# Optimization experiments

Hardware: AMD Instinct MI355X
Metric: run time of the kernel (lower is better)

The kernel has to match this reference:

```python
import jax, jax.numpy as jnp
import numpy as np

N_TREES, DEPTH, INPUT_DIM, N_CLASSES = 15, 3, 128, 10
N_LEAVES = 2 ** DEPTH
N_INTERNAL = N_LEAVES - 1


def _path_masks(depth):
    """Right/left ancestor indicator matrices [n_leaves, n_internal]."""
    n_leaves = 2 ** depth
    n_int = n_leaves - 1
    R = np.zeros((n_leaves, n_int), np.float32)
    L = np.zeros((n_leaves, n_int), np.float32)
    for leaf in range(n_leaves):
        node = leaf + n_int
        for _ in range(depth):
            parent = (node - 1) // 2
            if node % 2 == 0:
                R[leaf, parent] = 1.0
            else:
                L[leaf, parent] = 1.0
            node = parent
    return R, L

_R, _L = _path_masks(DEPTH)


def setup_inputs() -> dict:
    key = jax.random.key(0)
    k1, k2 = jax.random.split(key)
    batch = 262144
    per_tree = N_INTERNAL * INPUT_DIM + N_INTERNAL + N_LEAVES * N_CLASSES
    total = N_TREES * per_tree + N_TREES
    x = jax.random.normal(k1, (batch, INPUT_DIM), dtype=jnp.float32)
    params = jax.random.normal(k2, (total,), dtype=jnp.float32)
    return {"x": x, "params": params}


def reference(x, params):
    per_tree = N_INTERNAL * INPUT_DIM + N_INTERNAL + N_LEAVES * N_CLASSES
    blocks = params[: N_TREES * per_tree].reshape(N_TREES, per_tree)
    w_end = N_INTERNAL * INPUT_DIM
    split_w = blocks[:, :w_end].reshape(N_TREES, N_INTERNAL, INPUT_DIM)
    split_b = blocks[:, w_end : w_end + N_INTERNAL]  # [T, n_internal]
    leaf_logits = blocks[:, w_end + N_INTERNAL :].reshape(N_TREES, N_LEAVES, N_CLASSES)
    tree_w_logits = params[N_TREES * per_tree :]  # [T]

    # split logits z: [B, T, n_internal]
    z = jnp.einsum("bd,tnd->btn", x, split_w) + split_b[None, :, :]
    log_p = jax.nn.log_sigmoid(z)        # log sigma(z)
    log_1mp = jax.nn.log_sigmoid(-z)     # log (1 - sigma(z))

    R = jnp.asarray(_R)
    L = jnp.asarray(_L)
    # path product in log domain: [B, T, n_leaves]
    leaf_probs = jnp.exp(
        jnp.einsum("btn,ln->btl", log_p, R) + jnp.einsum("btn,ln->btl", log_1mp, L)
    )

    leaf_class_probs = jax.nn.softmax(leaf_logits, axis=-1)  # [T, n_leaves, C]
    tree_pred = jnp.einsum("btl,tlc->btc", leaf_probs, leaf_class_probs)
    tree_weights = jax.nn.softmax(tree_w_logits, axis=0)     # [T]
    final_pred = jnp.einsum("btc,t->bc", tree_pred, tree_weights)
    return final_pred
```

## Files before the change

kernel.cpp:

```cpp
#include <hip/hip_runtime.h>
#include <hip/hip_fp16.h>


typedef float    f32x4 __attribute__((ext_vector_type(4)));
typedef _Float16 half8 __attribute__((ext_vector_type(8)));

#define TREES      15
#define IDIM       128
#define NCLS       10
#define NINT       7
#define NLVS       8
#define PER_TREE   (NINT*IDIM + NINT + NLVS*NCLS)
#define NODES      (TREES*NINT)
#define NPAD       112
#define KPAD       128
#define RSTR       272
#define NBLK       512

__global__ __launch_bounds__(256) void prep_kernel(const float* __restrict__ p,
                                                   _Float16* __restrict__ wq,
                                                   float* __restrict__ bq,
                                                   _Float16* __restrict__ wbT) {
    const int gid  = blockIdx.x * 256 + threadIdx.x;
    const int nthr = gridDim.x * 256;

    for (int i = gid; i < NPAD * IDIM; i += nthr) {
        int g = i >> 7, k = i & 127;
        float v = 0.f;
        if (g < NODES) {
            int t = g / NINT, n = g % NINT;
            v = p[t * PER_TREE + n * IDIM + k];
        }
        wq[i] = (_Float16)v;
    }
    for (int i = gid; i < NPAD; i += nthr) {
        float v = 0.f;
        if (i < NODES) {
            int t = i / NINT, n = i % NINT;
            v = p[t * PER_TREE + NINT * IDIM + n];
        }
        bq[i] = v;
    }
    const float* tl = p + TREES * PER_TREE;
    for (int i = gid; i < 16 * KPAD; i += nthr) {
        int c = i >> 7, k = i & 127;
        float v = 0.f;
        if (c < NCLS && k < TREES * NLVS) {
            int t = k >> 3, l = k & 7;
            const float* ll = p + t * PER_TREE + NINT * IDIM + NINT + l * NCLS;
            float mx = ll[0];
            #pragma unroll
            for (int j = 1; j < NCLS; ++j) mx = fmaxf(mx, ll[j]);
            float se = 0.f;
            #pragma unroll
            for (int j = 0; j < NCLS; ++j) se += __expf(ll[j] - mx);
            float lsm = __expf(ll[c] - mx) / se;

            float m2 = tl[0];
            #pragma unroll
            for (int j = 1; j < TREES; ++j) m2 = fmaxf(m2, tl[j]);
            float s2 = 0.f;
            #pragma unroll
            for (int j = 0; j < TREES; ++j) s2 += __expf(tl[j] - m2);
            float tw = __expf(tl[t] - m2) / s2;
            v = lsm * tw;
        }
        wbT[i] = (_Float16)v;
    }
}

__device__ __forceinline__ void dma_quarter(const float* __restrict__ x,
                                            long grow0, char* qdst, int lane) {
    const int slot = lane & 31;
    #pragma unroll
    for (int it = 0; it < 8; ++it) {
        int r   = 2 * it + (lane >> 5);
        int c16 = (slot - r) & 31;
        const float* gp = x + (grow0 + r) * IDIM + c16 * 4;
        __builtin_amdgcn_global_load_lds(
            (const __attribute__((address_space(1))) void*)gp,
            (__attribute__((address_space(3))) void*)(qdst + it * 1024),
            16, 0, 0);
    }
}

__global__ __launch_bounds__(256, 2) void tree_main(const float* __restrict__ x,
                                                    const _Float16* __restrict__ wq,
                                                    const float* __restrict__ bq,
                                                    const _Float16* __restrict__ wbT,
                                                    float* __restrict__ out,
                                                    int tpb) {
    __shared__ __align__(16) char lds[2][32768];

    const int tid  = threadIdx.x;
    const int lane = tid & 63;
    const int w    = tid >> 6;
    const int lm   = lane & 15;
    const int lq   = lane >> 4;
    const int rg   = lane >> 2;
    const int g    = lane & 3;

    const long tile0 = (long)blockIdx.x * tpb;

    dma_quarter(x, tile0 * 64 + 16 * w, &lds[0][w * 8192], lane);

    half8 bf[7][4];
    float bb[7];
    #pragma unroll
    for (int nt = 0; nt < 7; ++nt) {
        bb[nt] = bq[16 * nt + lm];
        #pragma unroll
        for (int s = 0; s < 4; ++s)
            bf[nt][s] = *reinterpret_cast<const half8*>(wq + (16 * nt + lm) * IDIM + 32 * s + 8 * lq);
    }
    half8 wbf[4];
    #pragma unroll
    for (int s = 0; s < 4; ++s)
        wbf[s] = *reinterpret_cast<const half8*>(wbT + lm * KPAD + 32 * s + 8 * lq);

    for (int i = 0; i < tpb; ++i) {
        char* qcur = &lds[i & 1][w * 8192];
        const long grow = (tile0 + i) * 64;

        asm volatile("" ::: "memory");
        __builtin_amdgcn_s_waitcnt(0x0F70);
        asm volatile("" ::: "memory");

        half8 af[4];
        #pragma unroll
        for (int s = 0; s < 4; ++s) {
            int cc = 8 * s + 2 * lq;
            f32x4 f0 = *(const f32x4*)(qcur + lm * 512 + (((cc     + lm) & 31) << 4));
            f32x4 f1 = *(const f32x4*)(qcur + lm * 512 + (((cc + 1 + lm) & 31) << 4));
            half8 a;
            #pragma unroll
            for (int j = 0; j < 4; ++j) {
                a[j]     = (_Float16)f0[j];
                a[j + 4] = (_Float16)f1[j];
            }
            af[s] = a;
        }

        if (i + 1 < tpb)
            dma_quarter(x, (tile0 + i + 1) * 64 + 16 * w, &lds[(i + 1) & 1][w * 8192], lane);

        #pragma unroll
        for (int nt = 0; nt < 7; ++nt) {
            f32x4 acc = {0.f, 0.f, 0.f, 0.f};
            #pragma unroll
            for (int s = 0; s < 4; ++s)
                acc = __builtin_amdgcn_mfma_f32_16x16x32_f16(af[s], bf[nt][s], acc, 0, 0, 0);
            int node = 16 * nt + lm;
            int col  = node + ((node * 9363) >> 16);
            #pragma unroll
            for (int r = 0; r < 4; ++r) {
                float z  = acc[r] + bb[nt];
                float sg = __builtin_amdgcn_rcpf(1.0f + __expf(-z));
                *(_Float16*)(qcur + (4 * lq + r) * RSTR + col * 2) = (_Float16)sg;
            }
        }

        {
            const char* rowp = qcur + rg * RSTR;
            float sgv[4][7];
            #pragma unroll
            for (int tt = 0; tt < 4; ++tt) {
                int t = 4 * g + tt;
                #pragma unroll
                for (int n = 0; n < 7; ++n)
                    sgv[tt][n] = (float)*(const _Float16*)(rowp + (8 * t + n) * 2);
            }
            half8 lv[4];
            #pragma unroll
            for (int tt = 0; tt < 4; ++tt) {
                float s0 = sgv[tt][0], s1 = sgv[tt][1], s2 = sgv[tt][2];
                float s3 = sgv[tt][3], s4 = sgv[tt][4], s5 = sgv[tt][5], s6 = sgv[tt][6];
                float u1 = 1.f - s0, u2 = s0;
                float q1 = u1 * s1, q0 = u1 - q1;
                float q3 = u2 * s2, q2 = u2 - q3;
                float L1 = q0 * s3, L0 = q0 - L1;
                float L3 = q1 * s4, L2 = q1 - L3;
                float L5 = q2 * s5, L4 = q2 - L5;
                float L7 = q3 * s6, L6 = q3 - L7;
                float m = (4 * g + tt < TREES) ? 1.f : 0.f;
                half8 lv8;
                lv8[0] = (_Float16)(L0 * m); lv8[1] = (_Float16)(L1 * m);
                lv8[2] = (_Float16)(L2 * m); lv8[3] = (_Float16)(L3 * m);
                lv8[4] = (_Float16)(L4 * m); lv8[5] = (_Float16)(L5 * m);
                lv8[6] = (_Float16)(L6 * m); lv8[7] = (_Float16)(L7 * m);
                lv[tt] = lv8;
            }
            #pragma unroll
            for (int tt = 0; tt < 4; ++tt)
                *(half8*)(qcur + rg * RSTR + 64 * g + 16 * tt) = lv[tt];
        }

        {
            half8 af2[4];
            #pragma unroll
            for (int s = 0; s < 4; ++s)
                af2[s] = *(const half8*)(qcur + lm * RSTR + 64 * s + 16 * lq);
            f32x4 a2 = {0.f, 0.f, 0.f, 0.f};
            #pragma unroll
            for (int s = 0; s < 4; ++s)
                a2 = __builtin_amdgcn_mfma_f32_16x16x32_f16(af2[s], wbf[s], a2, 0, 0, 0);
            if (lm < NCLS) {
                #pragma unroll
                for (int r = 0; r < 4; ++r)
                    out[(grow + 16 * w + 4 * lq + r) * NCLS + lm] = a2[r];
            }
        }
    }
}

extern "C" void kernel_launch(void* const* d_in, const int* in_sizes, int n_in,
                              void* d_out, int out_size, void* d_ws, size_t ws_size,
                              hipStream_t stream) {
    const float* x      = (const float*)d_in[0];
    const float* params = (const float*)d_in[1];
    float* out = (float*)d_out;

    _Float16* wq  = (_Float16*)d_ws;
    float*    bq  = (float*)((char*)d_ws + NPAD * IDIM * 2);
    _Float16* wbT = (_Float16*)((char*)bq + NPAD * 4);

    const int batch = in_sizes[0] / IDIM;
    const int tiles = batch / 64;
    const int tpb   = tiles / NBLK;

    prep_kernel<<<8, 256, 0, stream>>>(params, wq, bq, wbT);
    tree_main<<<NBLK, 256, 0, stream>>>(x, wq, bq, wbT, out, tpb);
}
```

Before: 204.4 us.

## Fuse parameter prep into main kernel and relax per-tile waitcnt

New measurement: 304.1 us. 1.49x slower.

```diff
diff --git a/kernel.cpp b/kernel.cpp
--- a/kernel.cpp
+++ b/kernel.cpp
@@ -12,62 +12,8 @@
 #define NLVS       8
 #define PER_TREE   (NINT*IDIM + NINT + NLVS*NCLS)
 #define NODES      (TREES*NINT)
-#define NPAD       112
-#define KPAD       128
 #define RSTR       272
 #define NBLK       512
-
-__global__ __launch_bounds__(256) void prep_kernel(const float* __restrict__ p,
-                                                   _Float16* __restrict__ wq,
-                                                   float* __restrict__ bq,
-                                                   _Float16* __restrict__ wbT) {
-    const int gid  = blockIdx.x * 256 + threadIdx.x;
-    const int nthr = gridDim.x * 256;
-
-    for (int i = gid; i < NPAD * IDIM; i += nthr) {
-        int g = i >> 7, k = i & 127;
-        float v = 0.f;
-        if (g < NODES) {
-            int t = g / NINT, n = g % NINT;
-            v = p[t * PER_TREE + n * IDIM + k];
-        }
-        wq[i] = (_Float16)v;
-    }
-    for (int i = gid; i < NPAD; i += nthr) {
-        float v = 0.f;
-        if (i < NODES) {
-            int t = i / NINT, n = i % NINT;
-            v = p[t * PER_TREE + NINT * IDIM + n];
-        }
-        bq[i] = v;
-    }
-    const float* tl = p + TREES * PER_TREE;
-    for (int i = gid; i < 16 * KPAD; i += nthr) {
-        int c = i >> 7, k = i & 127;
-        float v = 0.f;
-        if (c < NCLS && k < TREES * NLVS) {
-            int t = k >> 3, l = k & 7;
-            const float* ll = p + t * PER_TREE + NINT * IDIM + NINT + l * NCLS;
-            float mx = ll[0];
-            #pragma unroll
-            for (int j = 1; j < NCLS; ++j) mx = fmaxf(mx, ll[j]);
-            float se = 0.f;
-            #pragma unroll
-            for (int j = 0; j < NCLS; ++j) se += __expf(ll[j] - mx);
-            float lsm = __expf(ll[c] - mx) / se;
-
-            float m2 = tl[0];
-            #pragma unroll
-            for (int j = 1; j < TREES; ++j) m2 = fmaxf(m2, tl[j]);
-            float s2 = 0.f;
-            #pragma unroll
-            for (int j = 0; j < TREES; ++j) s2 += __expf(tl[j] - m2);
-            float tw = __expf(tl[t] - m2) / s2;
-            v = lsm * tw;
-        }
-        wbT[i] = (_Float16)v;
-    }
-}
 
 __device__ __forceinline__ void dma_quarter(const float* __restrict__ x,
                                             long grow0, char* qdst, int lane) {
@@ -85,9 +31,7 @@
 }
 
 __global__ __launch_bounds__(256, 2) void tree_main(const float* __restrict__ x,
-                                                    const _Float16* __restrict__ wq,
-                                                    const float* __restrict__ bq,
-                                                    const _Float16* __restrict__ wbT,
+                                                    const float* __restrict__ p,
                                                     float* __restrict__ out,
                                                     int tpb) {
     __shared__ __align__(16) char lds[2][32768];
@@ -108,22 +52,64 @@
     float bb[7];
     #pragma unroll
     for (int nt = 0; nt < 7; ++nt) {
-        bb[nt] = bq[16 * nt + lm];
-        #pragma unroll
-        for (int s = 0; s < 4; ++s)
-            bf[nt][s] = *reinterpret_cast<const half8*>(wq + (16 * nt + lm) * IDIM + 32 * s + 8 * lq);
-    }
+        const int   node = 16 * nt + lm;
+        const float sc   = (node < NODES) ? 1.f : 0.f;
+        const int   nd   = (node < NODES) ? node : 0;
+        const int   t    = (nd * 9363) >> 16;
+        const int   n    = nd - 7 * t;
+        const float* wp  = p + t * PER_TREE + n * IDIM + 8 * lq;
+        #pragma unroll
+        for (int s = 0; s < 4; ++s) {
+            half8 h;
+            #pragma unroll
+            for (int j = 0; j < 8; ++j)
+                h[j] = (_Float16)(sc * wp[32 * s + j]);
+            bf[nt][s] = h;
+        }
+        bb[nt] = sc * p[t * PER_TREE + NINT * IDIM + n];
+    }
+
+    const float* tl = p + TREES * PER_TREE;
+    float m2 = tl[0];
+    #pragma unroll
+    for (int j = 1; j < TREES; ++j) m2 = fmaxf(m2, tl[j]);
+    float s2 = 0.f;
+    #pragma unroll
+    for (int j = 0; j < TREES; ++j) s2 += __expf(tl[j] - m2);
+
     half8 wbf[4];
     #pragma unroll
-    for (int s = 0; s < 4; ++s)
-        wbf[s] = *reinterpret_cast<const half8*>(wbT + lm * KPAD + 32 * s + 8 * lq);
+    for (int s = 0; s < 4; ++s) {
+        const int   t     = 4 * s + lq;
+        const int   tc    = (t < TREES) ? t : 0;
+        const float tmask = (t < TREES) ? 1.f : 0.f;
+        const float tw    = tmask * (__expf(tl[tc] - m2) / s2);
+        const int   cc    = (lm < NCLS) ? lm : 0;
+        const float cmask = (lm < NCLS) ? 1.f : 0.f;
+        const float* lb   = p + tc * PER_TREE + NINT * IDIM + NINT;
+        half8 hh;
+        #pragma unroll
+        for (int l = 0; l < NLVS; ++l) {
+            const float* ll = lb + l * NCLS;
+            float mx = ll[0];
+            #pragma unroll
+            for (int j = 1; j < NCLS; ++j) mx = fmaxf(mx, ll[j]);
+            float se = 0.f;
+            #pragma unroll
+            for (int j = 0; j < NCLS; ++j) se += __expf(ll[j] - mx);
+            float lsm = __expf(ll[cc] - mx) / se;
+            hh[l] = (_Float16)(lsm * tw * cmask);
+        }
+        wbf[s] = hh;
+    }
 
     for (int i = 0; i < tpb; ++i) {
         char* qcur = &lds[i & 1][w * 8192];
         const long grow = (tile0 + i) * 64;
 
         asm volatile("" ::: "memory");
-        __builtin_amdgcn_s_waitcnt(0x0F70);
+        if (i == 0) __builtin_amdgcn_s_waitcnt(0x0F70);
+        else        __builtin_amdgcn_s_waitcnt(0x0F74);
         asm volatile("" ::: "memory");
 
         half8 af[4];
@@ -146,7 +132,7 @@
 
         #pragma unroll
         for (int nt = 0; nt < 7; ++nt) {
-            f32x4 acc = {0.f, 0.f, 0.f, 0.f};
+            f32x4 acc = {bb[nt], bb[nt], bb[nt], bb[nt]};
             #pragma unroll
             for (int s = 0; s < 4; ++s)
                 acc = __builtin_amdgcn_mfma_f32_16x16x32_f16(af[s], bf[nt][s], acc, 0, 0, 0);
@@ -154,7 +140,7 @@
             int col  = node + ((node * 9363) >> 16);
             #pragma unroll
             for (int r = 0; r < 4; ++r) {
-                float z  = acc[r] + bb[nt];
+                float z  = acc[r];
                 float sg = __builtin_amdgcn_rcpf(1.0f + __expf(-z));
                 *(_Float16*)(qcur + (4 * lq + r) * RSTR + col * 2) = (_Float16)sg;
             }
@@ -162,22 +148,19 @@
 
         {
             const char* rowp = qcur + rg * RSTR;
-            float sgv[4][7];
+            half8 hv[4];
+            #pragma unroll
+            for (int tt = 0; tt < 4; ++tt)
+                hv[tt] = *(const half8*)(rowp + 64 * g + 16 * tt);
+            half8 lv[4];
             #pragma unroll
             for (int tt = 0; tt < 4; ++tt) {
-                int t = 4 * g + tt;
-                #pragma unroll
-                for (int n = 0; n < 7; ++n)
-                    sgv[tt][n] = (float)*(const _Float16*)(rowp + (8 * t + n) * 2);
-            }
-            half8 lv[4];
-            #pragma unroll
-            for (int tt = 0; tt < 4; ++tt) {
-                float s0 = sgv[tt][0], s1 = sgv[tt][1], s2 = sgv[tt][2];
-                float s3 = sgv[tt][3], s4 = sgv[tt][4], s5 = sgv[tt][5], s6 = sgv[tt][6];
+                float s0 = (float)hv[tt][0], s1 = (float)hv[tt][1], s2v = (float)hv[tt][2];
+                float s3 = (float)hv[tt][3], s4 = (float)hv[tt][4], s5 = (float)hv[tt][5];
+                float s6 = (float)hv[tt][6];
                 float u1 = 1.f - s0, u2 = s0;
                 float q1 = u1 * s1, q0 = u1 - q1;
-                float q3 = u2 * s2, q2 = u2 - q3;
+                float q3 = u2 * s2v, q2 = u2 - q3;
                 float L1 = q0 * s3, L0 = q0 - L1;
                 float L3 = q1 * s4, L2 = q1 - L3;
                 float L5 = q2 * s5, L4 = q2 - L5;
@@ -220,14 +203,9 @@
     const float* params = (const float*)d_in[1];
     float* out = (float*)d_out;
 
-    _Float16* wq  = (_Float16*)d_ws;
-    float*    bq  = (float*)((char*)d_ws + NPAD * IDIM * 2);
-    _Float16* wbT = (_Float16*)((char*)bq + NPAD * 4);
-
     const int batch = in_sizes[0] / IDIM;
     const int tiles = batch / 64;
     const int tpb   = tiles / NBLK;
 
-    prep_kernel<<<8, 256, 0, stream>>>(params, wq, bq, wbT);
-    tree_main<<<NBLK, 256, 0, stream>>>(x, wq, bq, wbT, out, tpb);
+    tree_main<<<NBLK, 256, 0, stream>>>(x, params, out, tpb);
 }
```
